# Kernel optimization log

Measured on AMD Instinct MI355X. Metric: run time of the kernel, lower is better.

The kernel has to match this reference:

```python
import jax, jax.numpy as jnp
import numpy as np

EPS = 0.3
LAYERS = 2


def setup_inputs() -> dict:
    key = jax.random.key(0)
    ks = jax.random.split(key, 8)
    N, F, H, C, E = 50000, 512, 128, 40, 800000

    def xavier(k, shape):
        fan_out, fan_in = shape[0], shape[-1]
        std = 1.414 * np.sqrt(2.0 / (fan_in + fan_out))
        return (jax.random.normal(k, shape, jnp.float32) * std).astype(jnp.float32)

    return {
        "x": jax.random.normal(ks[0], (N, F), jnp.float32),
        "t1_w": xavier(ks[1], (H, F)),
        "t1_b": jnp.zeros((H,), jnp.float32),
        "t2_w": xavier(ks[2], (C, H)),
        "t2_b": jnp.zeros((C,), jnp.float32),
        "gate_w": xavier(ks[3], (LAYERS, 2 * H)),  # Linear(2H,1) weight per layer
        "gate_b": jnp.zeros((LAYERS,), jnp.float32),
        "edge_index": jax.random.randint(ks[4], (2, E), 0, N, jnp.int32),
    }


def reference(x, t1_w, t1_b, t2_w, t2_b, gate_w, gate_b, edge_index):
    N = x.shape[0]
    H = t1_w.shape[0]
    row, col = edge_index[0], edge_index[1]  # source, target

    # norm_degree = degree(row).clamp(min=1) ** -0.5
    deg = jax.ops.segment_sum(jnp.ones_like(row, dtype=x.dtype), row, num_segments=N)
    nd = jnp.clip(deg, 1.0) ** -0.5  # [N]
    nd_r, nd_c = nd[row], nd[col]    # [E]

    # dropout is identity in eval mode
    h = jax.nn.relu(x @ t1_w.T + t1_b)  # [N,H]
    raw = h
    for l in range(LAYERS):
        h_src = h[row]  # x_j, [E,H]
        h_dst = h[col]  # [E,H]
        # gate(cat([h[row], h[col]])) == h_src @ W[:H] + h_dst @ W[H:] + b
        g = jnp.tanh(h_src @ gate_w[l, :H] + h_dst @ gate_w[l, H:] + gate_b[l])  # [E]
        norm = g * nd_r * nd_c  # [E]
        agg = jax.ops.segment_sum(norm[:, None] * h_src, col, num_segments=N)  # scatter-add at targets
        h = EPS * raw + agg
    out = h @ t2_w.T + t2_b  # [N,C]
    return jax.nn.log_softmax(out, axis=1)
```

## Files before the change

kernel.cpp:

```cpp
#include <hip/hip_runtime.h>
#include <math.h>

#define F_DIM 512
#define H_DIM 128
#define C_DIM 40
#define EPS_F 0.3f
#define NBLK 256

typedef float f32x4 __attribute__((ext_vector_type(4)));
typedef unsigned int u32x4 __attribute__((ext_vector_type(4)));
typedef __bf16 bf16x8 __attribute__((ext_vector_type(8)));
typedef unsigned short ushort_t;
typedef unsigned char uchar_t;

__device__ inline float bflo(unsigned t) { return __builtin_bit_cast(float, t << 16); }
__device__ inline float bfhi(unsigned t) { return __builtin_bit_cast(float, t & 0xffff0000u); }
__device__ inline unsigned short f2bf(float f) {
  unsigned u = __builtin_bit_cast(unsigned, f);
  u = (u + 0x7fffu + ((u >> 16) & 1u)) >> 16;
  return (unsigned short)u;
}
__device__ inline unsigned pack2bf(float a, float b) {
  unsigned ua = __builtin_bit_cast(unsigned, a);
  unsigned ub = __builtin_bit_cast(unsigned, b);
  ua = (ua + 0x7fffu + ((ua >> 16) & 1u)) >> 16;
  ub = (ub + 0x7fffu + ((ub >> 16) & 1u)) >> 16;
  return ua | (ub << 16);
}
__device__ inline float fast_tanh(float x) {
  float e = __expf(2.0f * x);
  return 1.0f - 2.0f / (e + 1.0f);
}


__global__ __launch_bounds__(256) void part_count(const int* __restrict__ row,
    const int* __restrict__ col, int* __restrict__ blkhist, int E, int nbkt, int chunk) {
  __shared__ int ch[256], rh[256];
  int t = threadIdx.x, b = blockIdx.x;
  ch[t] = 0; rh[t] = 0;
  __syncthreads();
  int s = b * chunk, e = min(E, s + chunk);
  for (int i = s + t; i < e; i += 256) {
    atomicAdd(&ch[((unsigned)col[i]) >> 8], 1);
    atomicAdd(&rh[((unsigned)row[i]) >> 8], 1);
  }
  __syncthreads();
  if (t < nbkt) {
    blkhist[t * NBLK + b] = ch[t];
    blkhist[(nbkt + t) * NBLK + b] = rh[t];
  }
}

__global__ __launch_bounds__(256) void part_scatter(const int* __restrict__ row,
    const int* __restrict__ col, const int* __restrict__ blkhist,
    int* __restrict__ bktbase, unsigned* __restrict__ colpart,
    uchar_t* __restrict__ rowpart, int E, int nbkt, int chunk) {
  __shared__ int sbase[400];
  __shared__ int stot[400];
  __shared__ int psum[256];
  __shared__ int sc[400];
  __shared__ int coff[400];
  int t = threadIdx.x, b = blockIdx.x;
  int nrows = 2 * nbkt;
  for (int rr = t; rr < nrows; rr += 256) {
    const int* rp = &blkhist[rr * NBLK];
    int pre = 0, tot = 0;
    for (int i = 0; i < NBLK; ++i) {
      int v = rp[i];
      pre += (i < b) ? v : 0;
      tot += v;
    }
    sbase[rr] = pre; stot[rr] = tot;
  }
  __syncthreads();
  int e0 = (2 * t     < nrows) ? stot[2 * t]     : 0;
  int e1 = (2 * t + 1 < nrows) ? stot[2 * t + 1] : 0;
  psum[t] = e0 + e1;
  __syncthreads();
  for (int off = 1; off < 256; off <<= 1) {
    int add = (t >= off) ? psum[t - off] : 0;
    __syncthreads();
    psum[t] += add;
    __syncthreads();
  }
  int pex = (t == 0) ? 0 : psum[t - 1];
  if (2 * t < nrows)     sc[2 * t]     = pex + sbase[2 * t];
  if (2 * t + 1 < nrows) sc[2 * t + 1] = pex + e0 + sbase[2 * t + 1];
  if (b == 0) {
    if (2 * t < nrows)     bktbase[2 * t]     = pex;
    if (2 * t + 1 < nrows) bktbase[2 * t + 1] = pex + e0;
    if (t == 0) bktbase[nrows] = 2 * E;
  }
  for (int rr = t; rr < nrows; rr += 256) coff[rr] = 0;
  __syncthreads();
  int s = b * chunk, e = min(E, s + chunk);
  for (int i = s + t; i < e; i += 256) {
    unsigned c = (unsigned)col[i], r = (unsigned)row[i];
    int bc = (int)(c >> 8), br = (int)(r >> 8);
    int pc = sc[bc] + atomicAdd(&coff[bc], 1);
    colpart[pc] = (r << 8) | (c & 255u);
    int pr = sc[nbkt + br] + atomicAdd(&coff[nbkt + br], 1) - E;
    rowpart[pr] = (uchar_t)(r & 255u);
  }
}

__global__ __launch_bounds__(256) void bucket_both(const unsigned* __restrict__ colpart,
    const uchar_t* __restrict__ rowpart, const int* __restrict__ bktbase,
    int* __restrict__ col_ptr, int* __restrict__ csr_src, float* __restrict__ nd,
    int N, int E, int nbkt) {
  __shared__ int cnt[256], ex[256], off[256];
  int t = threadIdx.x, bb = blockIdx.x;
  if (bb < nbkt) {
    int bkt = bb;
    int s = bktbase[bkt], e = bktbase[bkt + 1];
    cnt[t] = 0; off[t] = 0;
    __syncthreads();
    for (int i = s + t; i < e; i += 256)
      atomicAdd(&cnt[(int)(colpart[i] & 255u)], 1);
    __syncthreads();
    ex[t] = cnt[t];
    __syncthreads();
    for (int o = 1; o < 256; o <<= 1) {
      int v = (t >= o) ? ex[t - o] : 0;
      __syncthreads();
      ex[t] += v;
      __syncthreads();
    }
    int excl = (t == 0) ? 0 : ex[t - 1];
    __syncthreads();
    ex[t] = excl;
    __syncthreads();
    int node = bkt * 256 + t;
    if (node < N) col_ptr[node] = s + ex[t];
    if (bkt == 0 && t == 0) col_ptr[N] = E;
    for (int i = s + t; i < e; i += 256) {
      unsigned p = colpart[i];
      int lb = (int)(p & 255u);
      int dst = s + ex[lb] + atomicAdd(&off[lb], 1);
      csr_src[dst] = (int)(p >> 8);
    }
  } else {
    int bkt = bb - nbkt;
    int s = bktbase[nbkt + bkt] - E, e = bktbase[nbkt + bkt + 1] - E;
    cnt[t] = 0;
    __syncthreads();
    for (int i = s + t; i < e; i += 256)
      atomicAdd(&cnt[(int)rowpart[i]], 1);
    __syncthreads();
    int node = bkt * 256 + t;
    if (node < N) {
      int d = cnt[t] < 1 ? 1 : cnt[t];
      nd[node] = 1.0f / sqrtf((float)d);
    }
  }
}


__global__ __launch_bounds__(256) void gemm1_mfma(const float* __restrict__ x,
    const float* __restrict__ w, const float* __restrict__ b,
    const float* __restrict__ gwl, const float* __restrict__ gb,
    const float* __restrict__ nd,
    ushort_t* __restrict__ hbf, float2* __restrict__ pack0,
    float* __restrict__ s2a, int N) {
  __shared__ u32x4 AsBuf[1024];
  __shared__ u32x4 BsBuf[1024];
  char* Asc = (char*)AsBuf;
  char* Bsc = (char*)BsBuf;

  int t = threadIdx.x;
  int lane = t & 63;
  int wid = t >> 6;
  int wm = wid >> 1;
  int wn = wid & 1;
  int m0 = blockIdx.x * 128;
  int ql = lane & 15;

  f32x4 acc[4][4];
#pragma unroll
  for (int i = 0; i < 4; ++i)
#pragma unroll
    for (int j = 0; j < 4; ++j) acc[i][j] = (f32x4){0.f, 0.f, 0.f, 0.f};

  float bias[4], g1v[4], g2v[4];
#pragma unroll
  for (int j = 0; j < 4; ++j) {
    int c = wn * 64 + j * 16 + ql;
    bias[j] = b[c];
    g1v[j] = gwl[c];
    g2v[j] = gwl[H_DIM + c];
  }

  for (int kk = 0; kk < F_DIM; kk += 64) {
#pragma unroll
    for (int q = 0; q < 4; ++q) {
      int c = q * 256 + t;
      int row = c >> 3, kc = c & 7;
      int gm = m0 + row;
      f32x4 v0 = {0.f, 0.f, 0.f, 0.f}, v1 = {0.f, 0.f, 0.f, 0.f};
      if (gm < N) {
        const float* src = &x[(size_t)gm * F_DIM + kk + kc * 8];
        v0 = *(const f32x4*)src;
        v1 = *(const f32x4*)(src + 4);
      }
      u32x4 pk;
      pk[0] = pack2bf(v0[0], v0[1]);
      pk[1] = pack2bf(v0[2], v0[3]);
      pk[2] = pack2bf(v1[0], v1[1]);
      pk[3] = pack2bf(v1[2], v1[3]);
      *(u32x4*)(Asc + row * 128 + ((kc ^ (row & 7)) << 4)) = pk;
    }
#pragma unroll
    for (int q = 0; q < 4; ++q) {
      int c = q * 256 + t;
      int row = c >> 3, kc = c & 7;
      const float* src = &w[(size_t)row * F_DIM + kk + kc * 8];
      f32x4 v0 = *(const f32x4*)src;
      f32x4 v1 = *(const f32x4*)(src + 4);
      u32x4 pk;
      pk[0] = pack2bf(v0[0], v0[1]);
      pk[1] = pack2bf(v0[2], v0[3]);
      pk[2] = pack2bf(v1[0], v1[1]);
      pk[3] = pack2bf(v1[2], v1[3]);
      *(u32x4*)(Bsc + row * 128 + ((kc ^ (row & 7)) << 4)) = pk;
    }
    __syncthreads();
#pragma unroll
    for (int kh = 0; kh < 2; ++kh) {
      bf16x8 af[4], bfr[4];
      int kc = kh * 4 + (lane >> 4);
#pragma unroll
      for (int i = 0; i < 4; ++i) {
        int row = wm * 64 + i * 16 + ql;
        af[i] = *(const bf16x8*)(Asc + row * 128 + ((kc ^ (row & 7)) << 4));
      }
#pragma unroll
      for (int j = 0; j < 4; ++j) {
        int row = wn * 64 + j * 16 + ql;
        bfr[j] = *(const bf16x8*)(Bsc + row * 128 + ((kc ^ (row & 7)) << 4));
      }
#pragma unroll
      for (int i = 0; i < 4; ++i)
#pragma unroll
        for (int j = 0; j < 4; ++j)
          acc[i][j] = __builtin_amdgcn_mfma_f32_16x16x32_bf16(af[i], bfr[j], acc[i][j], 0, 0, 0);
    }
    __syncthreads();
  }

  float gp1[4][4], gp2[4][4];
#pragma unroll
  for (int i = 0; i < 4; ++i)
#pragma unroll
    for (int r = 0; r < 4; ++r) { gp1[i][r] = 0.f; gp2[i][r] = 0.f; }

#pragma unroll
  for (int i = 0; i < 4; ++i) {
    int rbase = m0 + wm * 64 + i * 16 + ((lane >> 4) * 4);
#pragma unroll
    for (int j = 0; j < 4; ++j) {
      int col = wn * 64 + j * 16 + ql;
#pragma unroll
      for (int r = 0; r < 4; ++r) {
        int gr = rbase + r;
        float o = fmaxf(acc[i][j][r] + bias[j], 0.f);
        if (gr < N) hbf[(size_t)gr * H_DIM + col] = f2bf(o);
        gp1[i][r] = fmaf(o, g1v[j], gp1[i][r]);
        gp2[i][r] = fmaf(o, g2v[j], gp2[i][r]);
      }
    }
  }
#pragma unroll
  for (int i = 0; i < 4; ++i)
#pragma unroll
    for (int r = 0; r < 4; ++r) {
#pragma unroll
      for (int m = 1; m < 16; m <<= 1) {
        gp1[i][r] += __shfl_xor(gp1[i][r], m);
        gp2[i][r] += __shfl_xor(gp2[i][r], m);
      }
    }
  float* pgA = (float*)AsBuf;
  float* pgB = (float*)AsBuf + 256;
  if (ql == 0) {
#pragma unroll
    for (int i = 0; i < 4; ++i)
#pragma unroll
      for (int r = 0; r < 4; ++r) {
        int lr = wm * 64 + i * 16 + (lane >> 4) * 4 + r;
        pgA[lr * 2 + wn] = gp1[i][r];
        pgB[lr * 2 + wn] = gp2[i][r];
      }
  }
  __syncthreads();
  if (t < 128) {
    int gr = m0 + t;
    if (gr < N) {
      float p1 = pgA[t * 2] + pgA[t * 2 + 1];
      float p2 = pgB[t * 2] + pgB[t * 2 + 1];
      float ndv = nd[gr];
      pack0[gr] = make_float2(p1, ndv);
      s2a[gr] = p2 + gb[0];
    }
  }
}


#define AGG_CORE(HSRC)                                                          \
  float ax = 0.f, ay = 0.f;                                                     \
  {                                                                             \
    int p0 = col_ptr[v], p1v = col_ptr[v + 1];                                  \
    float s2v = s2pb[v];                                                        \
    for (int base = p0; base < p1v; base += 64) {                               \
      int idx = base + lane;                                                    \
      int u = 0;                                                                \
      float cf = 0.f;                                                           \
      if (idx < p1v) {                                                          \
        u = csr_src[idx];                                                       \
        float2 pk = pack[u];                                                    \
        cf = fast_tanh(pk.x + s2v) * pk.y * ndv;                                \
      }                                                                         \
      int cnt = p1v - base;                                                     \
      if (cnt > 64) cnt = 64;                                                   \
      int j = 0;                                                                \
      for (; j + 8 <= cnt; j += 8) {                                            \
        int u0 = __shfl(u, j + 0), u1 = __shfl(u, j + 1);                       \
        int u2 = __shfl(u, j + 2), u3 = __shfl(u, j + 3);                       \
        int u4 = __shfl(u, j + 4), u5 = __shfl(u, j + 5);                       \
        int u6 = __shfl(u, j + 6), u7 = __shfl(u, j + 7);                       \
        unsigned t0 = *(const unsigned*)&HSRC[(size_t)u0 * H_DIM + lane * 2];   \
        unsigned t1 = *(const unsigned*)&HSRC[(size_t)u1 * H_DIM + lane * 2];   \
        unsigned t2 = *(const unsigned*)&HSRC[(size_t)u2 * H_DIM + lane * 2];   \
        unsigned t3 = *(const unsigned*)&HSRC[(size_t)u3 * H_DIM + lane * 2];   \
        unsigned t4 = *(const unsigned*)&HSRC[(size_t)u4 * H_DIM + lane * 2];   \
        unsigned t5 = *(const unsigned*)&HSRC[(size_t)u5 * H_DIM + lane * 2];   \
        unsigned t6 = *(const unsigned*)&HSRC[(size_t)u6 * H_DIM + lane * 2];   \
        unsigned t7 = *(const unsigned*)&HSRC[(size_t)u7 * H_DIM + lane * 2];   \
        float c0 = __shfl(cf, j + 0), c1 = __shfl(cf, j + 1);                   \
        float c2 = __shfl(cf, j + 2), c3 = __shfl(cf, j + 3);                   \
        float c4 = __shfl(cf, j + 4), c5 = __shfl(cf, j + 5);                   \
        float c6 = __shfl(cf, j + 6), c7 = __shfl(cf, j + 7);                   \
        ax = fmaf(c0, bflo(t0), ax); ay = fmaf(c0, bfhi(t0), ay);               \
        ax = fmaf(c1, bflo(t1), ax); ay = fmaf(c1, bfhi(t1), ay);               \
        ax = fmaf(c2, bflo(t2), ax); ay = fmaf(c2, bfhi(t2), ay);               \
        ax = fmaf(c3, bflo(t3), ax); ay = fmaf(c3, bfhi(t3), ay);               \
        ax = fmaf(c4, bflo(t4), ax); ay = fmaf(c4, bfhi(t4), ay);               \
        ax = fmaf(c5, bflo(t5), ax); ay = fmaf(c5, bfhi(t5), ay);               \
        ax = fmaf(c6, bflo(t6), ax); ay = fmaf(c6, bfhi(t6), ay);               \
        ax = fmaf(c7, bflo(t7), ax); ay = fmaf(c7, bfhi(t7), ay);               \
      }                                                                         \
      for (; j + 4 <= cnt; j += 4) {                                            \
        int u0 = __shfl(u, j + 0), u1 = __shfl(u, j + 1);                       \
        int u2 = __shfl(u, j + 2), u3 = __shfl(u, j + 3);                       \
        unsigned t0 = *(const unsigned*)&HSRC[(size_t)u0 * H_DIM + lane * 2];   \
        unsigned t1 = *(const unsigned*)&HSRC[(size_t)u1 * H_DIM + lane * 2];   \
        unsigned t2 = *(const unsigned*)&HSRC[(size_t)u2 * H_DIM + lane * 2];   \
        unsigned t3 = *(const unsigned*)&HSRC[(size_t)u3 * H_DIM + lane * 2];   \
        float c0 = __shfl(cf, j + 0), c1 = __shfl(cf, j + 1);                   \
        float c2 = __shfl(cf, j + 2), c3 = __shfl(cf, j + 3);                   \
        ax = fmaf(c0, bflo(t0), ax); ay = fmaf(c0, bfhi(t0), ay);               \
        ax = fmaf(c1, bflo(t1), ax); ay = fmaf(c1, bfhi(t1), ay);               \
        ax = fmaf(c2, bflo(t2), ax); ay = fmaf(c2, bfhi(t2), ay);               \
        ax = fmaf(c3, bflo(t3), ax); ay = fmaf(c3, bfhi(t3), ay);               \
      }                                                                         \
      for (; j < cnt; ++j) {                                                    \
        int uj = __shfl(u, j);                                                  \
        float cj = __shfl(cf, j);                                               \
        unsigned tj = *(const unsigned*)&HSRC[(size_t)uj * H_DIM + lane * 2];   \
        ax = fmaf(cj, bflo(tj), ax); ay = fmaf(cj, bfhi(tj), ay);               \
      }                                                                         \
    }                                                                           \
  }

__global__ __launch_bounds__(256) void agg1(const ushort_t* __restrict__ hbf,
    const float2* __restrict__ pack, const float* __restrict__ s2pb,
    const float* __restrict__ nd, const int* __restrict__ col_ptr,
    const int* __restrict__ csr_src, ushort_t* __restrict__ houtbf,
    const float* __restrict__ gwl, const float* __restrict__ gb1,
    float2* __restrict__ packo, float* __restrict__ s2o, int N) {
  int t = threadIdx.x;
  int v = blockIdx.x * 4 + (t >> 6);
  int lane = t & 63;
  if (v >= N) return;
  float ndv = nd[v];
  unsigned rv = *(const unsigned*)&hbf[(size_t)v * H_DIM + lane * 2];
  AGG_CORE(hbf)
  float ox = fmaf(EPS_F, bflo(rv), ax);
  float oy = fmaf(EPS_F, bfhi(rv), ay);
  *(unsigned*)&houtbf[(size_t)v * H_DIM + lane * 2] = pack2bf(ox, oy);
  float2 g1 = *(const float2*)&gwl[lane * 2];
  float2 g2 = *(const float2*)&gwl[H_DIM + lane * 2];
  float q1 = ox * g1.x + oy * g1.y;
  float q2 = ox * g2.x + oy * g2.y;
#pragma unroll
  for (int off = 32; off > 0; off >>= 1) {
    q1 += __shfl_xor(q1, off);
    q2 += __shfl_xor(q2, off);
  }
  if (lane == 0) {
    packo[v] = make_float2(q1, ndv);
    s2o[v] = q2 + gb1[0];
  }
}

__global__ __launch_bounds__(256) void agg2(const ushort_t* __restrict__ hbf,
    const ushort_t* __restrict__ rawbf, const float2* __restrict__ pack,
    const float* __restrict__ s2pb, const float* __restrict__ nd,
    const int* __restrict__ col_ptr, const int* __restrict__ csr_src,
    const float* __restrict__ w2, const float* __restrict__ b2,
    float* __restrict__ out, int N) {
  __shared__ float ws[C_DIM][129];
  __shared__ float bsh[C_DIM];
  __shared__ float hsm[4][H_DIM];
  int t = threadIdx.x;
  for (int i = t; i < C_DIM * H_DIM; i += 256) ws[i / H_DIM][i % H_DIM] = w2[i];
  if (t < C_DIM) bsh[t] = b2[t];
  __syncthreads();
  int wave = t >> 6, lane = t & 63;
  int v = blockIdx.x * 4 + wave;
  bool act = v < N;
  float ox = 0.f, oy = 0.f;
  if (act) {
    float ndv = nd[v];
    unsigned rv = *(const unsigned*)&rawbf[(size_t)v * H_DIM + lane * 2];
    AGG_CORE(hbf)
    ox = fmaf(EPS_F, bflo(rv), ax);
    oy = fmaf(EPS_F, bfhi(rv), ay);
    hsm[wave][lane * 2] = ox;
    hsm[wave][lane * 2 + 1] = oy;
  }
  __syncthreads();
  float accv = 0.f;
  if (act && lane < C_DIM) {
#pragma unroll 8
    for (int k = 0; k < H_DIM; ++k)
      accv = fmaf(hsm[wave][k], ws[lane][k], accv);
    accv += bsh[lane];
  }
  float m = (lane < C_DIM) ? accv : -1e30f;
#pragma unroll
  for (int off = 32; off > 0; off >>= 1) m = fmaxf(m, __shfl_xor(m, off));
  float ex = (lane < C_DIM) ? expf(accv - m) : 0.f;
  float s = ex;
#pragma unroll
  for (int off = 32; off > 0; off >>= 1) s += __shfl_xor(s, off);
  float lse = m + logf(s);
  if (act && lane < C_DIM) out[(size_t)v * C_DIM + lane] = accv - lse;
}


extern "C" void kernel_launch(void* const* d_in, const int* in_sizes, int n_in,
                              void* d_out, int out_size, void* d_ws, size_t ws_size,
                              hipStream_t stream) {
  const float* x   = (const float*)d_in[0];
  const float* t1w = (const float*)d_in[1];
  const float* t1b = (const float*)d_in[2];
  const float* t2w = (const float*)d_in[3];
  const float* t2b = (const float*)d_in[4];
  const float* gw  = (const float*)d_in[5];
  const float* gb  = (const float*)d_in[6];
  const int*   ei  = (const int*)d_in[7];
  const int N = in_sizes[0] / F_DIM;
  const int E = in_sizes[7] / 2;
  float* out = (float*)d_out;

  char* p = (char*)d_ws;
  auto take = [&](size_t bytes) {
    char* r = p;
    p += (bytes + 255) & ~(size_t)255;
    return r;
  };
  ushort_t* h0 = (ushort_t*)take((size_t)N * H_DIM * 2);
  ushort_t* h1 = (ushort_t*)take((size_t)N * H_DIM * 2);
  float2* pack0 = (float2*)take((size_t)N * 8);
  float2* pack1 = (float2*)take((size_t)N * 8);
  float* s2a = (float*)take((size_t)N * 4);
  float* s2b = (float*)take((size_t)N * 4);
  float* nd  = (float*)take((size_t)N * 4);
  int* col_ptr = (int*)take((size_t)(N + 1) * 4);
  int* csr_src = (int*)take((size_t)E * 4);

  const int nbkt = (N + 255) >> 8;
  const int chunk = (E + NBLK - 1) / NBLK;

  int* blkhist = (int*)take((size_t)2 * nbkt * NBLK * 4);
  int* bktbase = (int*)take((size_t)(2 * nbkt + 1) * 4);
  unsigned* colpart = (unsigned*)take((size_t)E * 4);
  uchar_t* rowpart  = (uchar_t*)take((size_t)E);

  const int* row = ei;
  const int* col = ei + E;

  part_count<<<NBLK, 256, 0, stream>>>(row, col, blkhist, E, nbkt, chunk);
  part_scatter<<<NBLK, 256, 0, stream>>>(row, col, blkhist, bktbase, colpart, rowpart, E, nbkt, chunk);
  bucket_both<<<2 * nbkt, 256, 0, stream>>>(colpart, rowpart, bktbase, col_ptr, csr_src, nd, N, E, nbkt);

  gemm1_mfma<<<(N + 127) / 128, 256, 0, stream>>>(x, t1w, t1b, gw, gb, nd, h0, pack0, s2a, N);

  int nwb = (N + 3) / 4;
  agg1<<<nwb, 256, 0, stream>>>(h0, pack0, s2a, nd, col_ptr, csr_src, h1,
                                gw + 2 * H_DIM, gb + 1, pack1, s2b, N);
  agg2<<<nwb, 256, 0, stream>>>(h1, h0, pack1, s2b, nd, col_ptr, csr_src,
                                t2w, t2b, out, N);
}
```

Measured before the change: 187.2 us.

## Precompute per-edge gate coefficients in a separate edge-parallel kernel

Adds a per-edge target array (16-bit node ids) built during CSR bucketing and a new edge-parallel kernel that computes the tanh gate times degree norms into a coef buffer before each aggregation layer. The aggregation kernels then just load coef instead of doing the pack gather and tanh inline, and broadcast with readlane instead of shfl. This moves the dependent pack gather and transcendental work off the latency-critical aggregation loop. The cost is two extra launches and an extra E-sized write and read. The ushort target id only holds node ids up to 65535, which fits N=50000.

```diff
diff --git a/kernel.cpp b/kernel.cpp
--- a/kernel.cpp
+++ b/kernel.cpp
@@ -31,6 +31,8 @@
   float e = __expf(2.0f * x);
   return 1.0f - 2.0f / (e + 1.0f);
 }
+#define RL(x, k)  __builtin_amdgcn_readlane((x), (k))
+#define RLF(x, k) __builtin_bit_cast(float, __builtin_amdgcn_readlane(__builtin_bit_cast(int, (x)), (k)))
 
 
 __global__ __launch_bounds__(256) void part_count(const int* __restrict__ row,
@@ -106,8 +108,8 @@
 
 __global__ __launch_bounds__(256) void bucket_both(const unsigned* __restrict__ colpart,
     const uchar_t* __restrict__ rowpart, const int* __restrict__ bktbase,
-    int* __restrict__ col_ptr, int* __restrict__ csr_src, float* __restrict__ nd,
-    int N, int E, int nbkt) {
+    int* __restrict__ col_ptr, int* __restrict__ csr_src, ushort_t* __restrict__ tgt,
+    float* __restrict__ nd, int N, int E, int nbkt) {
   __shared__ int cnt[256], ex[256], off[256];
   int t = threadIdx.x, bb = blockIdx.x;
   if (bb < nbkt) {
@@ -138,6 +140,7 @@
       int lb = (int)(p & 255u);
       int dst = s + ex[lb] + atomicAdd(&off[lb], 1);
       csr_src[dst] = (int)(p >> 8);
+      tgt[dst] = (ushort_t)(bkt * 256 + lb);
     }
   } else {
     int bkt = bb - nbkt;
@@ -305,83 +308,88 @@
 }
 
 
-#define AGG_CORE(HSRC)                                                          \
-  float ax = 0.f, ay = 0.f;                                                     \
-  {                                                                             \
-    int p0 = col_ptr[v], p1v = col_ptr[v + 1];                                  \
-    float s2v = s2pb[v];                                                        \
-    for (int base = p0; base < p1v; base += 64) {                               \
-      int idx = base + lane;                                                    \
-      int u = 0;                                                                \
-      float cf = 0.f;                                                           \
-      if (idx < p1v) {                                                          \
-        u = csr_src[idx];                                                       \
-        float2 pk = pack[u];                                                    \
-        cf = fast_tanh(pk.x + s2v) * pk.y * ndv;                                \
-      }                                                                         \
-      int cnt = p1v - base;                                                     \
-      if (cnt > 64) cnt = 64;                                                   \
-      int j = 0;                                                                \
-      for (; j + 8 <= cnt; j += 8) {                                            \
-        int u0 = __shfl(u, j + 0), u1 = __shfl(u, j + 1);                       \
-        int u2 = __shfl(u, j + 2), u3 = __shfl(u, j + 3);                       \
-        int u4 = __shfl(u, j + 4), u5 = __shfl(u, j + 5);                       \
-        int u6 = __shfl(u, j + 6), u7 = __shfl(u, j + 7);                       \
-        unsigned t0 = *(const unsigned*)&HSRC[(size_t)u0 * H_DIM + lane * 2];   \
-        unsigned t1 = *(const unsigned*)&HSRC[(size_t)u1 * H_DIM + lane * 2];   \
-        unsigned t2 = *(const unsigned*)&HSRC[(size_t)u2 * H_DIM + lane * 2];   \
-        unsigned t3 = *(const unsigned*)&HSRC[(size_t)u3 * H_DIM + lane * 2];   \
-        unsigned t4 = *(const unsigned*)&HSRC[(size_t)u4 * H_DIM + lane * 2];   \
-        unsigned t5 = *(const unsigned*)&HSRC[(size_t)u5 * H_DIM + lane * 2];   \
-        unsigned t6 = *(const unsigned*)&HSRC[(size_t)u6 * H_DIM + lane * 2];   \
-        unsigned t7 = *(const unsigned*)&HSRC[(size_t)u7 * H_DIM + lane * 2];   \
-        float c0 = __shfl(cf, j + 0), c1 = __shfl(cf, j + 1);                   \
-        float c2 = __shfl(cf, j + 2), c3 = __shfl(cf, j + 3);                   \
-        float c4 = __shfl(cf, j + 4), c5 = __shfl(cf, j + 5);                   \
-        float c6 = __shfl(cf, j + 6), c7 = __shfl(cf, j + 7);                   \
-        ax = fmaf(c0, bflo(t0), ax); ay = fmaf(c0, bfhi(t0), ay);               \
-        ax = fmaf(c1, bflo(t1), ax); ay = fmaf(c1, bfhi(t1), ay);               \
-        ax = fmaf(c2, bflo(t2), ax); ay = fmaf(c2, bfhi(t2), ay);               \
-        ax = fmaf(c3, bflo(t3), ax); ay = fmaf(c3, bfhi(t3), ay);               \
-        ax = fmaf(c4, bflo(t4), ax); ay = fmaf(c4, bfhi(t4), ay);               \
-        ax = fmaf(c5, bflo(t5), ax); ay = fmaf(c5, bfhi(t5), ay);               \
-        ax = fmaf(c6, bflo(t6), ax); ay = fmaf(c6, bfhi(t6), ay);               \
-        ax = fmaf(c7, bflo(t7), ax); ay = fmaf(c7, bfhi(t7), ay);               \
-      }                                                                         \
-      for (; j + 4 <= cnt; j += 4) {                                            \
-        int u0 = __shfl(u, j + 0), u1 = __shfl(u, j + 1);                       \
-        int u2 = __shfl(u, j + 2), u3 = __shfl(u, j + 3);                       \
-        unsigned t0 = *(const unsigned*)&HSRC[(size_t)u0 * H_DIM + lane * 2];   \
-        unsigned t1 = *(const unsigned*)&HSRC[(size_t)u1 * H_DIM + lane * 2];   \
-        unsigned t2 = *(const unsigned*)&HSRC[(size_t)u2 * H_DIM + lane * 2];   \
-        unsigned t3 = *(const unsigned*)&HSRC[(size_t)u3 * H_DIM + lane * 2];   \
-        float c0 = __shfl(cf, j + 0), c1 = __shfl(cf, j + 1);                   \
-        float c2 = __shfl(cf, j + 2), c3 = __shfl(cf, j + 3);                   \
-        ax = fmaf(c0, bflo(t0), ax); ay = fmaf(c0, bfhi(t0), ay);               \
-        ax = fmaf(c1, bflo(t1), ax); ay = fmaf(c1, bfhi(t1), ay);               \
-        ax = fmaf(c2, bflo(t2), ax); ay = fmaf(c2, bfhi(t2), ay);               \
-        ax = fmaf(c3, bflo(t3), ax); ay = fmaf(c3, bfhi(t3), ay);               \
-      }                                                                         \
-      for (; j < cnt; ++j) {                                                    \
-        int uj = __shfl(u, j);                                                  \
-        float cj = __shfl(cf, j);                                               \
-        unsigned tj = *(const unsigned*)&HSRC[(size_t)uj * H_DIM + lane * 2];   \
-        ax = fmaf(cj, bflo(tj), ax); ay = fmaf(cj, bfhi(tj), ay);               \
-      }                                                                         \
-    }                                                                           \
+__global__ __launch_bounds__(256) void coef_kernel(const int* __restrict__ csr_src,
+    const ushort_t* __restrict__ tgt, const float2* __restrict__ pack,
+    const float* __restrict__ s2pb, const float* __restrict__ ndarr,
+    float* __restrict__ coef, int E) {
+  int i = blockIdx.x * 256 + threadIdx.x;
+  if (i >= E) return;
+  int u = csr_src[i];
+  int v = (int)tgt[i];
+  float2 pk = pack[u];
+  coef[i] = fast_tanh(pk.x + s2pb[v]) * pk.y * ndarr[v];
+}
+
+
+#define GBODY(K)                                                               \
+  {                                                                            \
+    int u_##K = RL(u, j + K);                                                  \
+    const ushort_t* r_##K = HSRC_ + (size_t)u_##K * H_DIM;                     \
+    tv[K] = *(const unsigned*)(r_##K + lane * 2);                              \
+  }
+
+#define AGG_CORE(HSRC)                                                         \
+  float ax = 0.f, ay = 0.f;                                                    \
+  {                                                                            \
+    const ushort_t* HSRC_ = (HSRC);                                            \
+    int p0 = col_ptr[v], p1v = col_ptr[v + 1];                                 \
+    for (int base = p0; base < p1v; base += 64) {                              \
+      int idx = base + lane;                                                   \
+      int u = 0;                                                               \
+      float cf = 0.f;                                                          \
+      if (idx < p1v) {                                                         \
+        u = csr_src[idx];                                                      \
+        cf = coef[idx];                                                        \
+      }                                                                        \
+      int cnt = p1v - base;                                                    \
+      if (cnt > 64) cnt = 64;                                                  \
+      int j = 0;                                                               \
+      for (; j + 8 <= cnt; j += 8) {                                           \
+        unsigned tv[8];                                                        \
+        GBODY(0) GBODY(1) GBODY(2) GBODY(3)                                    \
+        GBODY(4) GBODY(5) GBODY(6) GBODY(7)                                    \
+        float c0 = RLF(cf, j + 0), c1 = RLF(cf, j + 1);                        \
+        float c2 = RLF(cf, j + 2), c3 = RLF(cf, j + 3);                        \
+        float c4 = RLF(cf, j + 4), c5 = RLF(cf, j + 5);                        \
+        float c6 = RLF(cf, j + 6), c7 = RLF(cf, j + 7);                        \
+        ax = fmaf(c0, bflo(tv[0]), ax); ay = fmaf(c0, bfhi(tv[0]), ay);        \
+        ax = fmaf(c1, bflo(tv[1]), ax); ay = fmaf(c1, bfhi(tv[1]), ay);        \
+        ax = fmaf(c2, bflo(tv[2]), ax); ay = fmaf(c2, bfhi(tv[2]), ay);        \
+        ax = fmaf(c3, bflo(tv[3]), ax); ay = fmaf(c3, bfhi(tv[3]), ay);        \
+        ax = fmaf(c4, bflo(tv[4]), ax); ay = fmaf(c4, bfhi(tv[4]), ay);        \
+        ax = fmaf(c5, bflo(tv[5]), ax); ay = fmaf(c5, bfhi(tv[5]), ay);        \
+        ax = fmaf(c6, bflo(tv[6]), ax); ay = fmaf(c6, bfhi(tv[6]), ay);        \
+        ax = fmaf(c7, bflo(tv[7]), ax); ay = fmaf(c7, bfhi(tv[7]), ay);        \
+      }                                                                        \
+      for (; j + 4 <= cnt; j += 4) {                                           \
+        unsigned tv[4];                                                        \
+        GBODY(0) GBODY(1) GBODY(2) GBODY(3)                                    \
+        float c0 = RLF(cf, j + 0), c1 = RLF(cf, j + 1);                        \
+        float c2 = RLF(cf, j + 2), c3 = RLF(cf, j + 3);                        \
+        ax = fmaf(c0, bflo(tv[0]), ax); ay = fmaf(c0, bfhi(tv[0]), ay);        \
+        ax = fmaf(c1, bflo(tv[1]), ax); ay = fmaf(c1, bfhi(tv[1]), ay);        \
+        ax = fmaf(c2, bflo(tv[2]), ax); ay = fmaf(c2, bfhi(tv[2]), ay);        \
+        ax = fmaf(c3, bflo(tv[3]), ax); ay = fmaf(c3, bfhi(tv[3]), ay);        \
+      }                                                                        \
+      for (; j < cnt; ++j) {                                                   \
+        int uj = RL(u, j);                                                     \
+        float cj = RLF(cf, j);                                                 \
+        unsigned tj = *(const unsigned*)(HSRC_ + (size_t)uj * H_DIM + lane * 2);\
+        ax = fmaf(cj, bflo(tj), ax); ay = fmaf(cj, bfhi(tj), ay);              \
+      }                                                                        \
+    }                                                                          \
   }
 
 __global__ __launch_bounds__(256) void agg1(const ushort_t* __restrict__ hbf,
-    const float2* __restrict__ pack, const float* __restrict__ s2pb,
-    const float* __restrict__ nd, const int* __restrict__ col_ptr,
-    const int* __restrict__ csr_src, ushort_t* __restrict__ houtbf,
+    const float* __restrict__ coef, const int* __restrict__ col_ptr,
+    const int* __restrict__ csr_src, const float* __restrict__ nd,
+    ushort_t* __restrict__ houtbf,
     const float* __restrict__ gwl, const float* __restrict__ gb1,
     float2* __restrict__ packo, float* __restrict__ s2o, int N) {
   int t = threadIdx.x;
   int v = blockIdx.x * 4 + (t >> 6);
   int lane = t & 63;
   if (v >= N) return;
-  float ndv = nd[v];
   unsigned rv = *(const unsigned*)&hbf[(size_t)v * H_DIM + lane * 2];
   AGG_CORE(hbf)
   float ox = fmaf(EPS_F, bflo(rv), ax);
@@ -397,14 +405,13 @@
     q2 += __shfl_xor(q2, off);
   }
   if (lane == 0) {
-    packo[v] = make_float2(q1, ndv);
+    packo[v] = make_float2(q1, nd[v]);
     s2o[v] = q2 + gb1[0];
   }
 }
 
 __global__ __launch_bounds__(256) void agg2(const ushort_t* __restrict__ hbf,
-    const ushort_t* __restrict__ rawbf, const float2* __restrict__ pack,
-    const float* __restrict__ s2pb, const float* __restrict__ nd,
+    const ushort_t* __restrict__ rawbf, const float* __restrict__ coef,
     const int* __restrict__ col_ptr, const int* __restrict__ csr_src,
     const float* __restrict__ w2, const float* __restrict__ b2,
     float* __restrict__ out, int N) {
@@ -418,13 +425,11 @@
   int wave = t >> 6, lane = t & 63;
   int v = blockIdx.x * 4 + wave;
   bool act = v < N;
-  float ox = 0.f, oy = 0.f;
   if (act) {
-    float ndv = nd[v];
     unsigned rv = *(const unsigned*)&rawbf[(size_t)v * H_DIM + lane * 2];
     AGG_CORE(hbf)
-    ox = fmaf(EPS_F, bflo(rv), ax);
-    oy = fmaf(EPS_F, bfhi(rv), ay);
+    float ox = fmaf(EPS_F, bflo(rv), ax);
+    float oy = fmaf(EPS_F, bfhi(rv), ay);
     hsm[wave][lane * 2] = ox;
     hsm[wave][lane * 2 + 1] = oy;
   }
@@ -478,6 +483,8 @@
   float* nd  = (float*)take((size_t)N * 4);
   int* col_ptr = (int*)take((size_t)(N + 1) * 4);
   int* csr_src = (int*)take((size_t)E * 4);
+  ushort_t* tgt = (ushort_t*)take((size_t)E * 2);
+  float* coef = (float*)take((size_t)E * 4);
 
   const int nbkt = (N + 255) >> 8;
   const int chunk = (E + NBLK - 1) / NBLK;
@@ -492,13 +499,16 @@
 
   part_count<<<NBLK, 256, 0, stream>>>(row, col, blkhist, E, nbkt, chunk);
   part_scatter<<<NBLK, 256, 0, stream>>>(row, col, blkhist, bktbase, colpart, rowpart, E, nbkt, chunk);
-  bucket_both<<<2 * nbkt, 256, 0, stream>>>(colpart, rowpart, bktbase, col_ptr, csr_src, nd, N, E, nbkt);
+  bucket_both<<<2 * nbkt, 256, 0, stream>>>(colpart, rowpart, bktbase, col_ptr, csr_src, tgt, nd, N, E, nbkt);
 
   gemm1_mfma<<<(N + 127) / 128, 256, 0, stream>>>(x, t1w, t1b, gw, gb, nd, h0, pack0, s2a, N);
 
+  int ebl = (E + 255) / 256;
   int nwb = (N + 3) / 4;
-  agg1<<<nwb, 256, 0, stream>>>(h0, pack0, s2a, nd, col_ptr, csr_src, h1,
+  coef_kernel<<<ebl, 256, 0, stream>>>(csr_src, tgt, pack0, s2a, nd, coef, E);
+  agg1<<<nwb, 256, 0, stream>>>(h0, coef, col_ptr, csr_src, nd, h1,
                                 gw + 2 * H_DIM, gb + 1, pack1, s2b, N);
-  agg2<<<nwb, 256, 0, stream>>>(h1, h0, pack1, s2b, nd, col_ptr, csr_src,
+  coef_kernel<<<ebl, 256, 0, stream>>>(csr_src, tgt, pack1, s2b, nd, coef, E);
+  agg2<<<nwb, 256, 0, stream>>>(h1, h0, coef, col_ptr, csr_src,
                                 t2w, t2b, out, N);
 }
```

Result: slower. 195.2 us (+4.2%).
